# Kernel optimization log

Hardware: AMD Instinct MI355X
Metric: run time of the kernel (lower is better)

The kernel has to match this reference:

```python
import jax, jax.numpy as jnp
import numpy as np

B, L, D, H = 4, 1024, 1024, 16
DH = D // H
NEG = -1e9
EPS = 1e-5


def setup_inputs() -> dict:
    key = jax.random.key(0)
    ks = jax.random.split(key, 12)
    s = 1.0 / np.sqrt(D)
    inp = {
        "Q": jax.random.normal(ks[0], (B, L, D), jnp.float32),
        "K": jax.random.normal(ks[1], (B, L, D), jnp.float32),
        "V": jax.random.normal(ks[2], (B, L, D), jnp.float32),
        "K_mask": jnp.ones((B, L), jnp.int32),
        "WQ": jax.random.normal(ks[3], (D, D), jnp.float32) * s,
        "bQ": jnp.zeros((D,), jnp.float32),
        "WK": jax.random.normal(ks[4], (D, D), jnp.float32) * s,
        "bK": jnp.zeros((D,), jnp.float32),
        "WV": jax.random.normal(ks[5], (D, D), jnp.float32) * s,
        "bV": jnp.zeros((D,), jnp.float32),
        "WO": jax.random.normal(ks[6], (D, D), jnp.float32) * s,
        "bO": jnp.zeros((D,), jnp.float32),
        "ln_g": jnp.ones((D,), jnp.float32),
        "ln_b": jnp.zeros((D,), jnp.float32),
    }
    return inp


def _mha(Q, K, V, K_mask, WQ, bQ, WK, bK, WV, bV, WO, bO, ln_g, ln_b):
    # projections  [B,L,D]
    q = Q @ WQ + bQ
    k = K @ WK + bK
    v = V @ WV + bV
    # split heads -> [B,H,L,dh]
    q = q.reshape(B, L, H, DH).transpose(0, 2, 1, 3)
    k = k.reshape(B, L, H, DH).transpose(0, 2, 1, 3)
    v = v.reshape(B, L, H, DH).transpose(0, 2, 1, 3)
    # scaled dot product, masked softmax over keys
    scores = jnp.einsum("bhqd,bhkd->bhqk", q, k) / jnp.sqrt(jnp.float32(DH))
    mask = (K_mask > 0)[:, None, None, :]  # [B,1,1,Lk]
    scores = jnp.where(mask, scores, NEG)
    attn = jax.nn.softmax(scores, axis=-1)  # dropout is identity at inference
    ctx = jnp.einsum("bhqk,bhkd->bhqd", attn, v)
    ctx = ctx.transpose(0, 2, 1, 3).reshape(B, L, D)
    # output layer: dense + residual + layernorm
    out = ctx @ WO + bO
    x = out + Q
    mu = jnp.mean(x, axis=-1, keepdims=True)
    var = jnp.var(x, axis=-1, keepdims=True)
    return (x - mu) * jax.lax.rsqrt(var + EPS) * ln_g + ln_b


def reference(Q, K, V, K_mask, WQ, bQ, WK, bK, WV, bV, WO, bO, ln_g, ln_b):
    return _mha(Q, K, V, K_mask, WQ, bQ, WK, bK, WV, bV, WO, bO, ln_g, ln_b)
```

## Files before the change

### kernel.cpp

```cpp
#include <hip/hip_runtime.h>
#include <hip/hip_bf16.h>
#include <stdint.h>

#define Bn 4
#define Ln 1024
#define Dn 1024
#define Hn 16
#define DHn 64
#define Mn (Bn*Ln)

typedef __attribute__((ext_vector_type(8))) short short8v;
typedef __attribute__((ext_vector_type(4))) float floatx4;

__device__ __forceinline__ unsigned short f2b(float f){
  union { float f; unsigned u; } v; v.f = f;
  unsigned r = (v.u + 0x7FFFu + ((v.u >> 16) & 1u)) >> 16;
  return (unsigned short)r;
}
__device__ __forceinline__ unsigned short f2b_fast(float f){
  __hip_bfloat16 h = __float2bfloat16(f);
  return *reinterpret_cast<unsigned short*>(&h);
}

typedef const unsigned __attribute__((address_space(1)))* gas1_t;
typedef unsigned __attribute__((address_space(3)))* las3_t;
__device__ __forceinline__ void gload16(const void* g, void* l){
  __builtin_amdgcn_global_load_lds((gas1_t)(uintptr_t)g, (las3_t)(uintptr_t)l, 16, 0, 0);
}

__global__ __launch_bounds__(256) void prep_k(const float* __restrict__ W0,
    const float* __restrict__ W1, const float* __restrict__ W2,
    const float* __restrict__ W3, unsigned short* __restrict__ Wt0,
    unsigned short* __restrict__ Wt1, unsigned short* __restrict__ Wt2,
    unsigned short* __restrict__ Wt3, const float* __restrict__ x0,
    const float* __restrict__ x1, const float* __restrict__ x2,
    unsigned short* __restrict__ o0, unsigned short* __restrict__ o1,
    unsigned short* __restrict__ o2)
{
  __shared__ float tile[64][65];
  if (blockIdx.x < 1024){
    const int z = blockIdx.x >> 8, rem = blockIdx.x & 255;
    const float* W; unsigned short* Wt;
    switch (z){
      case 0: W = W0; Wt = Wt0; break;
      case 1: W = W1; Wt = Wt1; break;
      case 2: W = W2; Wt = Wt2; break;
      default: W = W3; Wt = Wt3; break;
    }
    const int nb = (rem & 15) * 64, kb = (rem >> 4) * 64;
    const int tx = threadIdx.x & 63, ty = threadIdx.x >> 6;
    #pragma unroll
    for (int r = 0; r < 64; r += 4)
      tile[r + ty][tx] = W[(size_t)(kb + r + ty) * 1024 + nb + tx];
    __syncthreads();
    #pragma unroll
    for (int r = 0; r < 64; r += 4)
      Wt[(size_t)(nb + r + ty) * 1024 + kb + tx] = f2b(tile[tx][r + ty]);
  } else {
    const int i = (blockIdx.x - 1024) * 256 + threadIdx.x;
    const int sel = i >> 20, idx = i & 0xFFFFF;
    const float* x = sel == 0 ? x0 : (sel == 1 ? x1 : x2);
    unsigned short* o = sel == 0 ? o0 : (sel == 1 ? o1 : o2);
    float4 v = reinterpret_cast<const float4*>(x)[idx];
    union { unsigned short u[4]; uint2 q; } p;
    p.u[0] = f2b(v.x); p.u[1] = f2b(v.y); p.u[2] = f2b(v.z); p.u[3] = f2b(v.w);
    reinterpret_cast<uint2*>(o)[idx] = p.q;
  }
}

template<int MODE>
__device__ __forceinline__ void gemm8_core(const unsigned short* __restrict__ Ab,
    const unsigned short* __restrict__ Btp, const float* __restrict__ bias,
    void* __restrict__ outp, float scale, unsigned short* lds, int nt, int mt)
{
  const int tid = threadIdx.x;
  const int lane = tid & 63, wave = tid >> 6;
  const int wr = wave >> 2, wc = wave & 3;
  const int lg = lane >> 4, lr = lane & 15;
  const int m0 = mt * 256, n0 = nt * 256;

  const unsigned short* gAb[2];
  const unsigned short* gBb[2];
  int ldso[2];
  #pragma unroll
  for (int i = 0; i < 2; i++){
    int c = tid + 512 * i;
    int g16 = c >> 6, lrr = c & 15, lgg = (c >> 4) & 3;
    int row = g16 * 16 + lrr;
    gAb[i] = Ab  + (size_t)(m0 + row) * 1024 + lgg * 8;
    gBb[i] = Btp + (size_t)(n0 + row) * 1024 + lgg * 8;
    ldso[i] = c * 8;
  }
  auto stageA = [&](int sg){
    unsigned short* slot = lds + (sg & 3) * 16384;
    const int kcol = (sg >> 1) * 64 + (sg & 1) * 32;
    #pragma unroll
    for (int i = 0; i < 2; i++) gload16(gAb[i] + kcol, &slot[ldso[i]]);
  };
  auto stageB = [&](int sg){
    unsigned short* slot = lds + (sg & 3) * 16384 + 8192;
    const int kcol = (sg >> 1) * 64 + (sg & 1) * 32;
    #pragma unroll
    for (int i = 0; i < 2; i++) gload16(gBb[i] + kcol, &slot[ldso[i]]);
  };

  floatx4 acc[8][4] = {};

  stageA(0); stageB(0); stageA(1); stageB(1); stageA(2); stageB(2);

  for (int t = 0; t < 16; t++){
    unsigned short* slot0 = lds + ((2 * t) & 3) * 16384;
    unsigned short* slot1 = lds + ((2 * t + 1) & 3) * 16384;
    short8v af[4], bf[4];
    if (t < 15) asm volatile("s_waitcnt vmcnt(4)" ::: "memory");
    else        asm volatile("s_waitcnt vmcnt(0)" ::: "memory");
    __builtin_amdgcn_s_barrier();
    __builtin_amdgcn_sched_barrier(0);
    if (t < 15) stageA(2 * t + 3);
    #pragma unroll
    for (int n = 0; n < 4; n++)
      bf[n] = *reinterpret_cast<const short8v*>(&slot0[8192 + ((wc * 4 + n) * 64 + lane) * 8]);
    #pragma unroll
    for (int i2 = 0; i2 < 4; i2++)
      af[i2] = *reinterpret_cast<const short8v*>(&slot0[((wr * 8 + i2) * 64 + lane) * 8]);
    __builtin_amdgcn_s_setprio(1);
    #pragma unroll
    for (int a = 0; a < 4; a++)
      #pragma unroll
      for (int n = 0; n < 4; n++)
        acc[a][n] = __builtin_amdgcn_mfma_f32_16x16x32_bf16(af[a], bf[n], acc[a][n], 0, 0, 0);
    __builtin_amdgcn_s_setprio(0);
    if (t < 15) stageB(2 * t + 3);
    #pragma unroll
    for (int i2 = 0; i2 < 4; i2++)
      af[i2] = *reinterpret_cast<const short8v*>(&slot0[((wr * 8 + 4 + i2) * 64 + lane) * 8]);
    __builtin_amdgcn_s_setprio(1);
    #pragma unroll
    for (int a = 0; a < 4; a++)
      #pragma unroll
      for (int n = 0; n < 4; n++)
        acc[4 + a][n] = __builtin_amdgcn_mfma_f32_16x16x32_bf16(af[a], bf[n], acc[4 + a][n], 0, 0, 0);
    __builtin_amdgcn_s_setprio(0);
    __builtin_amdgcn_sched_barrier(0);
    __builtin_amdgcn_s_barrier();
    __builtin_amdgcn_sched_barrier(0);
    if (t < 14) stageA(2 * t + 4);
    #pragma unroll
    for (int n = 0; n < 4; n++)
      bf[n] = *reinterpret_cast<const short8v*>(&slot1[8192 + ((wc * 4 + n) * 64 + lane) * 8]);
    #pragma unroll
    for (int i2 = 0; i2 < 4; i2++)
      af[i2] = *reinterpret_cast<const short8v*>(&slot1[((wr * 8 + i2) * 64 + lane) * 8]);
    __builtin_amdgcn_s_setprio(1);
    #pragma unroll
    for (int a = 0; a < 4; a++)
      #pragma unroll
      for (int n = 0; n < 4; n++)
        acc[a][n] = __builtin_amdgcn_mfma_f32_16x16x32_bf16(af[a], bf[n], acc[a][n], 0, 0, 0);
    __builtin_amdgcn_s_setprio(0);
    if (t < 14) stageB(2 * t + 4);
    #pragma unroll
    for (int i2 = 0; i2 < 4; i2++)
      af[i2] = *reinterpret_cast<const short8v*>(&slot1[((wr * 8 + 4 + i2) * 64 + lane) * 8]);
    __builtin_amdgcn_s_setprio(1);
    #pragma unroll
    for (int a = 0; a < 4; a++)
      #pragma unroll
      for (int n = 0; n < 4; n++)
        acc[4 + a][n] = __builtin_amdgcn_mfma_f32_16x16x32_bf16(af[a], bf[n], acc[4 + a][n], 0, 0, 0);
    __builtin_amdgcn_s_setprio(0);
    __builtin_amdgcn_sched_barrier(0);
  }

  if constexpr (MODE == 2){
    __syncthreads();
    #pragma unroll
    for (int n = 0; n < 4; n++){
      const int gn_l = wc * 64 + n * 16 + lr;
      const float bb = bias[n0 + gn_l];
      const int X = (gn_l & 7) << 3;
      #pragma unroll
      for (int a = 0; a < 8; a++){
        const int gm_l = wr * 128 + a * 16 + lg * 4;
        union { unsigned short u[4]; uint2 q; } pk;
        #pragma unroll
        for (int r = 0; r < 4; r++) pk.u[r] = f2b((acc[a][n][r] + bb) * scale);
        *reinterpret_cast<uint2*>(&lds[gn_l * 256 + (gm_l ^ X)]) = pk.q;
      }
    }
    __syncthreads();
    const int bb2 = m0 >> 10, l0 = m0 & 1023;
    const int row = tid >> 1, colb = (tid & 1) * 128;
    const int h2 = (n0 + row) >> 6, d = (n0 + row) & 63;
    unsigned short* obase = (unsigned short*)outp +
        (((size_t)(bb2 * Hn + h2)) * DHn + d) * Ln + l0 + colb;
    const int XR = (row & 7) << 3;
    #pragma unroll
    for (int g = 0; g < 16; g++){
      short8v v = *reinterpret_cast<const short8v*>(&lds[row * 256 + ((colb + g * 8) ^ XR)]);
      *reinterpret_cast<short8v*>(obase + g * 8) = v;
    }
  } else {
    unsigned short* plw = lds + wave * 1152;
    unsigned short* o = (unsigned short*)outp;
    const int gnb = n0 + wc * 64;
    const int h2 = gnb >> 6;
    float bb4[4];
    #pragma unroll
    for (int n = 0; n < 4; n++) bb4[n] = bias[gnb + n * 16 + lr];
    #pragma unroll
    for (int a = 0; a < 8; a++){
      #pragma unroll
      for (int n = 0; n < 4; n++)
        #pragma unroll
        for (int r = 0; r < 4; r++)
          plw[(lg * 4 + r) * 72 + n * 16 + lr] = f2b((acc[a][n][r] + bb4[n]) * scale);
      #pragma unroll
      for (int it = 0; it < 2; it++){
        const int row = it * 8 + (lane >> 3);
        const int c   = lane & 7;
        const int gm  = m0 + wr * 128 + a * 16 + row;
        const int b2 = gm >> 10, l = gm & 1023;
        short8v v = *reinterpret_cast<const short8v*>(&plw[row * 72 + c * 8]);
        *reinterpret_cast<short8v*>(o + (((size_t)(b2 * Hn + h2)) * Ln + l) * DHn + c * 8) = v;
      }
    }
  }
}

__global__ __launch_bounds__(512, 2) void gemmqkv8_k(
    const unsigned short* __restrict__ A0, const unsigned short* __restrict__ A1,
    const unsigned short* __restrict__ A2, const unsigned short* __restrict__ W0,
    const unsigned short* __restrict__ W1, const unsigned short* __restrict__ W2,
    const float* __restrict__ b0, const float* __restrict__ b1,
    const float* __restrict__ b2, unsigned short* __restrict__ o0,
    unsigned short* __restrict__ o1, unsigned short* __restrict__ o2, float qscl)
{
  __shared__ __align__(16) unsigned short lds[65536];
  const int g = blockIdx.x >> 3;
  const int nt = g & 3;
  const int panel = (g >> 2) * 8 + (blockIdx.x & 7);
  const int z = panel >> 4, mt = panel & 15;
  if (z == 0)
    gemm8_core<0>(A0, W0, b0, o0, qscl, lds, nt, mt);
  else if (z == 1)
    gemm8_core<0>(A1, W1, b1, o1, 1.f, lds, nt, mt);
  else
    gemm8_core<2>(A2, W2, b2, o2, 1.f, lds, nt, mt);
}

__global__ __launch_bounds__(256) void gemmo_k(const unsigned short* __restrict__ Ab,
    const unsigned short* __restrict__ W, const float* __restrict__ bias,
    float* __restrict__ out, const float* __restrict__ resid)
{
  __shared__ __align__(16) unsigned short lds[32768];
  const int bid = blockIdx.x;
  const int xcd = bid & 7, k = bid >> 3;
  const int mt = xcd * 4 + (k >> 3);
  const int nt = k & 7;

  const int tid = threadIdx.x;
  const int lane = tid & 63, wave = tid >> 6;
  const int wr = wave >> 1, wc = wave & 1;
  const int lg = lane >> 4, lr = lane & 15;
  const int m0 = mt * 128, n0 = nt * 128;

  const unsigned short* gA[2];
  const unsigned short* gB[2];
  int ldso[2];
  #pragma unroll
  for (int i = 0; i < 2; i++){
    int c = tid + 256 * i;
    int g16 = c >> 6, lrr = c & 15, lgg = (c >> 4) & 3;
    int row = g16 * 16 + lrr;
    gA[i] = Ab + (size_t)(m0 + row) * 1024 + lgg * 8;
    gB[i] = W  + (size_t)(n0 + row) * 1024 + lgg * 8;
    ldso[i] = c * 8;
  }
  auto issue = [&](int s){
    unsigned short* base = lds + (s & 3) * 8192;
    const int kc = s * 32;
    #pragma unroll
    for (int i = 0; i < 2; i++) gload16(gA[i] + kc, &base[ldso[i]]);
    #pragma unroll
    for (int i = 0; i < 2; i++) gload16(gB[i] + kc, &base[4096 + ldso[i]]);
  };

  floatx4 acc[4][4] = {};

  issue(0); issue(1); issue(2);

  for (int s = 0; s < 32; s++){
    unsigned short* base = lds + (s & 3) * 8192;
    if (s <= 29)      asm volatile("s_waitcnt vmcnt(8)" ::: "memory");
    else if (s == 30) asm volatile("s_waitcnt vmcnt(4)" ::: "memory");
    else              asm volatile("s_waitcnt vmcnt(0)" ::: "memory");
    __builtin_amdgcn_s_barrier();
    __builtin_amdgcn_sched_barrier(0);
    if (s <= 28) issue(s + 3);
    short8v af[4], bf[4];
    #pragma unroll
    for (int m = 0; m < 4; m++)
      af[m] = *reinterpret_cast<const short8v*>(&base[((wr * 4 + m) * 64 + lane) * 8]);
    #pragma unroll
    for (int n = 0; n < 4; n++)
      bf[n] = *reinterpret_cast<const short8v*>(&base[4096 + ((wc * 4 + n) * 64 + lane) * 8]);
    __builtin_amdgcn_s_setprio(1);
    #pragma unroll
    for (int m = 0; m < 4; m++)
      #pragma unroll
      for (int n = 0; n < 4; n++)
        acc[m][n] = __builtin_amdgcn_mfma_f32_16x16x32_bf16(af[m], bf[n], acc[m][n], 0, 0, 0);
    __builtin_amdgcn_s_setprio(0);
    __builtin_amdgcn_sched_barrier(0);
  }

  #pragma unroll
  for (int n = 0; n < 4; n++){
    const int gn = n0 + wc * 64 + n * 16 + lr;
    const float bb = bias[gn];
    #pragma unroll
    for (int m = 0; m < 4; m++){
      const int gm0 = m0 + wr * 64 + m * 16 + lg * 4;
      #pragma unroll
      for (int r = 0; r < 4; r++){
        const int gm = gm0 + r;
        out[(size_t)gm * Dn + gn] = acc[m][n][r] + bb + resid[(size_t)gm * Dn + gn];
      }
    }
  }
}

__global__ __launch_bounds__(256) void attn_k(const unsigned short* __restrict__ qb,
    const unsigned short* __restrict__ kbf, const unsigned short* __restrict__ vtb,
    const int* __restrict__ kmask, unsigned short* __restrict__ ctx)
{
  const int bh = blockIdx.x;
  const int qt = blockIdx.y;
  const int b = bh >> 4, h = bh & 15;
  const int tid = threadIdx.x;
  const int w = tid >> 6, lane = tid & 63;
  const int lg = lane >> 4, lr = lane & 15;

  const unsigned short* qp = qb  + (size_t)bh * Ln * DHn;
  const unsigned short* kp = kbf + (size_t)bh * Ln * DHn;
  const unsigned short* vp = vtb + (size_t)bh * DHn * Ln;
  const int q0 = qt * 128 + w * 32;

  __shared__ __align__(16) unsigned short ldsK[2][4096];
  __shared__ __align__(16) unsigned short ldsV[2][4096];
  __shared__ __align__(16) unsigned short plds[4][32][72];

  const unsigned short* gK[2];
  const unsigned short* gV[2];
  #pragma unroll
  for (int i = 0; i < 2; i++){
    int bc = w * 2 + i;
    int ks = bc >> 2, j = bc & 3;
    int row = j * 16 + lr, col = ks * 32 + lg * 8;
    gK[i] = kp + (size_t)row * DHn + col;
    gV[i] = vp + (size_t)row * Ln  + col;
  }

  short8v aq[2][2];
  #pragma unroll
  for (int f = 0; f < 2; f++)
    #pragma unroll
    for (int ks = 0; ks < 2; ks++)
      aq[f][ks] = *reinterpret_cast<const short8v*>(
          qp + (size_t)(q0 + f * 16 + lr) * DHn + ks * 32 + lg * 8);

  floatx4 accO[2][4] = {};
  float lsacc[2][4] = {{0.f,0.f,0.f,0.f},{0.f,0.f,0.f,0.f}};

  const int* mrow = kmask + b * Ln;
  int mkA[4], mkB[4];

  #pragma unroll
  for (int i = 0; i < 2; i++){
    gload16(gK[i], &ldsK[0][(w * 2 + i) * 512]);
    gload16(gV[i], &ldsV[0][(w * 2 + i) * 512]);
  }
  #pragma unroll
  for (int j = 0; j < 4; j++) mkA[j] = mrow[j * 16 + lr];

  for (int t = 0; t < 16; t++){
    const int cur = t & 1;
    asm volatile("s_waitcnt vmcnt(0)" ::: "memory");
    __syncthreads();
    if (t < 15){
      #pragma unroll
      for (int i = 0; i < 2; i++){
        gload16(gK[i] + (size_t)(t + 1) * 4096, &ldsK[cur ^ 1][(w * 2 + i) * 512]);
        gload16(gV[i] + (size_t)(t + 1) * 64,   &ldsV[cur ^ 1][(w * 2 + i) * 512]);
      }
      #pragma unroll
      for (int j = 0; j < 4; j++) mkB[j] = mrow[(t + 1) * 64 + j * 16 + lr];
    }

    floatx4 s[2][4] = {};
    #pragma unroll
    for (int ks = 0; ks < 2; ks++)
      #pragma unroll
      for (int j = 0; j < 4; j++){
        short8v bk = *reinterpret_cast<const short8v*>(&ldsK[cur][((ks * 4 + j) * 64 + lane) * 8]);
        s[0][j] = __builtin_amdgcn_mfma_f32_16x16x32_bf16(aq[0][ks], bk, s[0][j], 0, 0, 0);
        s[1][j] = __builtin_amdgcn_mfma_f32_16x16x32_bf16(aq[1][ks], bk, s[1][j], 0, 0, 0);
      }
    if (__all(mkA[0] > 0 && mkA[1] > 0 && mkA[2] > 0 && mkA[3] > 0)){
      #pragma unroll
      for (int f = 0; f < 2; f++)
        #pragma unroll
        for (int j = 0; j < 4; j++)
          #pragma unroll
          for (int r = 0; r < 4; r++){
            float p = __builtin_amdgcn_exp2f(s[f][j][r]);
            lsacc[f][r] += p;
            plds[w][f * 16 + lg * 4 + r][j * 16 + lr] = f2b_fast(p);
          }
    } else {
      #pragma unroll
      for (int j = 0; j < 4; j++){
        const float madd = mkA[j] > 0 ? 0.f : -1e9f;
        #pragma unroll
        for (int f = 0; f < 2; f++)
          #pragma unroll
          for (int r = 0; r < 4; r++){
            float p = __builtin_amdgcn_exp2f(s[f][j][r] + madd);
            lsacc[f][r] += p;
            plds[w][f * 16 + lg * 4 + r][j * 16 + lr] = f2b_fast(p);
          }
      }
    }
    #pragma unroll
    for (int ks = 0; ks < 2; ks++){
      short8v pa0 = *reinterpret_cast<const short8v*>(&plds[w][lr][ks * 32 + lg * 8]);
      short8v pa1 = *reinterpret_cast<const short8v*>(&plds[w][16 + lr][ks * 32 + lg * 8]);
      #pragma unroll
      for (int n = 0; n < 4; n++){
        short8v bv = *reinterpret_cast<const short8v*>(&ldsV[cur][((ks * 4 + n) * 64 + lane) * 8]);
        accO[0][n] = __builtin_amdgcn_mfma_f32_16x16x32_bf16(pa0, bv, accO[0][n], 0, 0, 0);
        accO[1][n] = __builtin_amdgcn_mfma_f32_16x16x32_bf16(pa1, bv, accO[1][n], 0, 0, 0);
      }
    }
    #pragma unroll
    for (int j = 0; j < 4; j++) mkA[j] = mkB[j];
  }

  #pragma unroll
  for (int f = 0; f < 2; f++)
    #pragma unroll
    for (int r = 0; r < 4; r++){
      lsacc[f][r] += __shfl_xor(lsacc[f][r], 1, 64);
      lsacc[f][r] += __shfl_xor(lsacc[f][r], 2, 64);
      lsacc[f][r] += __shfl_xor(lsacc[f][r], 4, 64);
      lsacc[f][r] += __shfl_xor(lsacc[f][r], 8, 64);
      lsacc[f][r] = 1.f / fmaxf(lsacc[f][r], 1e-20f);
    }
  #pragma unroll
  for (int f = 0; f < 2; f++)
    #pragma unroll
    for (int n = 0; n < 4; n++)
      #pragma unroll
      for (int r = 0; r < 4; r++)
        plds[w][f * 16 + lg * 4 + r][n * 16 + lr] = f2b_fast(accO[f][n][r] * lsacc[f][r]);
  #pragma unroll
  for (int it = 0; it < 4; it++){
    const int row = it * 8 + (lane >> 3);
    const int c = lane & 7;
    const int q = q0 + row;
    short8v v = *reinterpret_cast<const short8v*>(&plds[w][row][c * 8]);
    *reinterpret_cast<short8v*>(ctx + ((size_t)(b * Ln + q)) * Dn + h * DHn + c * 8) = v;
  }
}

__global__ __launch_bounds__(256) void ln_k(const float* __restrict__ x,
    const float* __restrict__ g, const float* __restrict__ bt, float* __restrict__ out)
{
  const int row = blockIdx.x;
  const int tid = threadIdx.x;
  float4 v = *reinterpret_cast<const float4*>(x + (size_t)row * 1024 + tid * 4);
  float s  = v.x + v.y + v.z + v.w;
  float sq = v.x * v.x + v.y * v.y + v.z * v.z + v.w * v.w;
  #pragma unroll
  for (int off = 32; off >= 1; off >>= 1){
    s  += __shfl_xor(s, off, 64);
    sq += __shfl_xor(sq, off, 64);
  }
  __shared__ float psm[4], pqm[4];
  const int w = tid >> 6;
  if ((tid & 63) == 0){ psm[w] = s; pqm[w] = sq; }
  __syncthreads();
  s  = psm[0] + psm[1] + psm[2] + psm[3];
  sq = pqm[0] + pqm[1] + pqm[2] + pqm[3];
  const float mean = s * (1.f / 1024.f);
  const float var  = sq * (1.f / 1024.f) - mean * mean;
  const float inv  = rsqrtf(var + 1e-5f);
  float4 gg = *reinterpret_cast<const float4*>(g  + tid * 4);
  float4 bb = *reinterpret_cast<const float4*>(bt + tid * 4);
  float4 o;
  o.x = (v.x - mean) * inv * gg.x + bb.x;
  o.y = (v.y - mean) * inv * gg.y + bb.y;
  o.z = (v.z - mean) * inv * gg.z + bb.z;
  o.w = (v.w - mean) * inv * gg.w + bb.w;
  *reinterpret_cast<float4*>(out + (size_t)row * 1024 + tid * 4) = o;
}

extern "C" void kernel_launch(void* const* d_in, const int* in_sizes, int n_in,
                              void* d_out, int out_size, void* d_ws, size_t ws_size,
                              hipStream_t stream)
{
  const float* Qin = (const float*)d_in[0];
  const float* Kin = (const float*)d_in[1];
  const float* Vin = (const float*)d_in[2];
  const int*   Kms = (const int*)d_in[3];
  const float* WQ  = (const float*)d_in[4];
  const float* bQ  = (const float*)d_in[5];
  const float* WK  = (const float*)d_in[6];
  const float* bK  = (const float*)d_in[7];
  const float* WV  = (const float*)d_in[8];
  const float* bV  = (const float*)d_in[9];
  const float* WO  = (const float*)d_in[10];
  const float* bO  = (const float*)d_in[11];
  const float* lng = (const float*)d_in[12];
  const float* lnb = (const float*)d_in[13];

  char* ws = (char*)d_ws;
  const size_t MB = 1024u * 1024u;
  unsigned short* wqt = (unsigned short*)(ws + 0 * MB);
  unsigned short* wkt = (unsigned short*)(ws + 2 * MB);
  unsigned short* wvt = (unsigned short*)(ws + 4 * MB);
  unsigned short* wot = (unsigned short*)(ws + 6 * MB);
  unsigned short* qbf = (unsigned short*)(ws + 8 * MB);
  unsigned short* kbf = (unsigned short*)(ws + 16 * MB);
  unsigned short* vtb = (unsigned short*)(ws + 24 * MB);
  unsigned short* ctx = (unsigned short*)(ws + 32 * MB);
  float*          xbf = (float*)(ws + 40 * MB);
  unsigned short* cv0 = (unsigned short*)(ws + 32 * MB);
  unsigned short* cv1 = (unsigned short*)(ws + 40 * MB);
  unsigned short* cv2 = (unsigned short*)(ws + 48 * MB);

  dim3 blk(256);
  prep_k<<<13312, blk, 0, stream>>>(WQ, WK, WV, WO, wqt, wkt, wvt, wot,
                                    Qin, Kin, Vin, cv0, cv1, cv2);

  const float QSCL = 0.125f * 1.44269504088896f;
  gemmqkv8_k<<<192, dim3(512), 0, stream>>>(cv0, cv1, cv2, wqt, wkt, wvt,
                                            bQ, bK, bV, qbf, kbf, vtb, QSCL);

  attn_k<<<dim3(64, 8), blk, 0, stream>>>(qbf, kbf, vtb, Kms, ctx);

  gemmo_k<<<256, blk, 0, stream>>>(ctx, wot, bO, xbf, Qin);

  ln_k<<<4096, blk, 0, stream>>>(xbf, lng, lnb, (float*)d_out);
}
```

Baseline: 118.1 us.

## Triple-buffer K/V tiles in attention and stage key mask in LDS

The attention kernel moves from double to triple buffering of the K and V tiles, issuing loads two iterations ahead and waiting with vmcnt(4) so one tile's loads stay in flight across the barrier. The key mask is loaded into LDS once at the start instead of per-iteration global loads into registers. This aims to hide global-load latency behind the MFMA work. The cost is more LDS per block (one extra 16 KB buffer set plus 4 KB for the mask), which may lower occupancy.

```diff
diff --git a/kernel.cpp b/kernel.cpp
--- a/kernel.cpp
+++ b/kernel.cpp
@@ -347,9 +347,18 @@
   const unsigned short* vp = vtb + (size_t)bh * DHn * Ln;
   const int q0 = qt * 128 + w * 32;
 
-  __shared__ __align__(16) unsigned short ldsK[2][4096];
-  __shared__ __align__(16) unsigned short ldsV[2][4096];
+  __shared__ __align__(16) unsigned short ldsK[3][4096];
+  __shared__ __align__(16) unsigned short ldsV[3][4096];
   __shared__ __align__(16) unsigned short plds[4][32][72];
+  __shared__ __align__(16) int ldsM[1024];
+
+  short8v aq[2][2];
+  #pragma unroll
+  for (int f = 0; f < 2; f++)
+    #pragma unroll
+    for (int ks = 0; ks < 2; ks++)
+      aq[f][ks] = *reinterpret_cast<const short8v*>(
+          qp + (size_t)(q0 + f * 16 + lr) * DHn + ks * 32 + lg * 8);
 
   const unsigned short* gK[2];
   const unsigned short* gV[2];
@@ -361,53 +370,46 @@
     gK[i] = kp + (size_t)row * DHn + col;
     gV[i] = vp + (size_t)row * Ln  + col;
   }
-
-  short8v aq[2][2];
-  #pragma unroll
-  for (int f = 0; f < 2; f++)
-    #pragma unroll
-    for (int ks = 0; ks < 2; ks++)
-      aq[f][ks] = *reinterpret_cast<const short8v*>(
-          qp + (size_t)(q0 + f * 16 + lr) * DHn + ks * 32 + lg * 8);
+  auto issue = [&](int t){
+    unsigned short* bK = ldsK[t % 3];
+    unsigned short* bV = ldsV[t % 3];
+    #pragma unroll
+    for (int i = 0; i < 2; i++){
+      gload16(gK[i] + (size_t)t * 4096, &bK[(w * 2 + i) * 512]);
+      gload16(gV[i] + (size_t)t * 64,   &bV[(w * 2 + i) * 512]);
+    }
+  };
 
   floatx4 accO[2][4] = {};
   float lsacc[2][4] = {{0.f,0.f,0.f,0.f},{0.f,0.f,0.f,0.f}};
 
-  const int* mrow = kmask + b * Ln;
-  int mkA[4], mkB[4];
-
-  #pragma unroll
-  for (int i = 0; i < 2; i++){
-    gload16(gK[i], &ldsK[0][(w * 2 + i) * 512]);
-    gload16(gV[i], &ldsV[0][(w * 2 + i) * 512]);
-  }
-  #pragma unroll
-  for (int j = 0; j < 4; j++) mkA[j] = mrow[j * 16 + lr];
+  gload16(kmask + b * Ln + w * 256 + lane * 4, &ldsM[w * 256]);
+  issue(0);
+  issue(1);
 
   for (int t = 0; t < 16; t++){
-    const int cur = t & 1;
-    asm volatile("s_waitcnt vmcnt(0)" ::: "memory");
-    __syncthreads();
-    if (t < 15){
-      #pragma unroll
-      for (int i = 0; i < 2; i++){
-        gload16(gK[i] + (size_t)(t + 1) * 4096, &ldsK[cur ^ 1][(w * 2 + i) * 512]);
-        gload16(gV[i] + (size_t)(t + 1) * 64,   &ldsV[cur ^ 1][(w * 2 + i) * 512]);
-      }
-      #pragma unroll
-      for (int j = 0; j < 4; j++) mkB[j] = mrow[(t + 1) * 64 + j * 16 + lr];
-    }
+    if (t < 15) asm volatile("s_waitcnt vmcnt(4)" ::: "memory");
+    else        asm volatile("s_waitcnt vmcnt(0)" ::: "memory");
+    __builtin_amdgcn_s_barrier();
+    __builtin_amdgcn_sched_barrier(0);
+    if (t < 14) issue(t + 2);
+
+    const unsigned short* bK = ldsK[t % 3];
+    const unsigned short* bV = ldsV[t % 3];
 
     floatx4 s[2][4] = {};
     #pragma unroll
     for (int ks = 0; ks < 2; ks++)
       #pragma unroll
       for (int j = 0; j < 4; j++){
-        short8v bk = *reinterpret_cast<const short8v*>(&ldsK[cur][((ks * 4 + j) * 64 + lane) * 8]);
+        short8v bk = *reinterpret_cast<const short8v*>(&bK[((ks * 4 + j) * 64 + lane) * 8]);
         s[0][j] = __builtin_amdgcn_mfma_f32_16x16x32_bf16(aq[0][ks], bk, s[0][j], 0, 0, 0);
         s[1][j] = __builtin_amdgcn_mfma_f32_16x16x32_bf16(aq[1][ks], bk, s[1][j], 0, 0, 0);
       }
-    if (__all(mkA[0] > 0 && mkA[1] > 0 && mkA[2] > 0 && mkA[3] > 0)){
+    int mk[4];
+    #pragma unroll
+    for (int j = 0; j < 4; j++) mk[j] = ldsM[t * 64 + j * 16 + lr];
+    if (__all(mk[0] > 0 && mk[1] > 0 && mk[2] > 0 && mk[3] > 0)){
       #pragma unroll
       for (int f = 0; f < 2; f++)
         #pragma unroll
@@ -421,7 +423,7 @@
     } else {
       #pragma unroll
       for (int j = 0; j < 4; j++){
-        const float madd = mkA[j] > 0 ? 0.f : -1e9f;
+        const float madd = mk[j] > 0 ? 0.f : -1e9f;
         #pragma unroll
         for (int f = 0; f < 2; f++)
           #pragma unroll
@@ -438,13 +440,11 @@
       short8v pa1 = *reinterpret_cast<const short8v*>(&plds[w][16 + lr][ks * 32 + lg * 8]);
       #pragma unroll
       for (int n = 0; n < 4; n++){
-        short8v bv = *reinterpret_cast<const short8v*>(&ldsV[cur][((ks * 4 + n) * 64 + lane) * 8]);
+        short8v bv = *reinterpret_cast<const short8v*>(&bV[((ks * 4 + n) * 64 + lane) * 8]);
         accO[0][n] = __builtin_amdgcn_mfma_f32_16x16x32_bf16(pa0, bv, accO[0][n], 0, 0, 0);
         accO[1][n] = __builtin_amdgcn_mfma_f32_16x16x32_bf16(pa1, bv, accO[1][n], 0, 0, 0);
       }
     }
-    #pragma unroll
-    for (int j = 0; j < 4; j++) mkA[j] = mkB[j];
   }
 
   #pragma unroll
```

Result: no change. 119.7 us (+1.4%).
